# Performance work log

Hardware: AMD Instinct MI355X
Metric: run time of the kernel (lower is better)

The kernel has to match this reference:

```python
import jax, jax.numpy as jnp
import numpy as np

B, S, N, M, D = 1, 8, 768, 768, 64
K, RATIO, IT, THR = 8, 0.6, 16, 0.75
R_N, R_M = int(RATIO * N), int(RATIO * M)


def _solver(sx, sy, sm):
    # mask-weighted cross-correlation model: (Bi, D, D)
    w = sm.astype(sx.dtype)
    num = jnp.einsum('bnd,bnm,bme->bde', sx, w, sy)
    den = jnp.sum(w, axis=(-2, -1))[:, None, None] + 1e-6
    return num / den


def _evaluator(models, x, y, mask):
    # squared L2 residual ||x @ model - y||^2, NaN where mask is False -> (Bi, N, M)
    xt = jnp.einsum('bnd,bde->bne', x, models)
    sq = (jnp.sum(xt * xt, -1)[:, :, None] + jnp.sum(y * y, -1)[:, None, :]
          - 2.0 * jnp.einsum('bne,bme->bnm', xt, y))
    return jnp.where(mask, sq, jnp.nan)


def _ransac(x, y, mask, perm1, perm2):
    Bi, n, d = x.shape
    m = y.shape[1]
    p1 = perm1.reshape(-1)  # (IT*R_N,) values in [0, R_N)
    p2 = perm2.reshape(-1)
    s_x = x[:, p1].reshape(Bi * IT, R_N, d)
    s_y = y[:, p2].reshape(Bi * IT, R_M, d)
    s_m = mask[:, p1].reshape(Bi, IT, R_N, m)
    s_m = jnp.take_along_axis(s_m, perm2[None, :, None, :], axis=-1)
    s_m = s_m.reshape(Bi * IT, R_N, R_M)
    models = _solver(s_x, s_y, s_m)  # (Bi*IT, D, D)
    xr = jnp.broadcast_to(x[:, None], (Bi, IT, n, d)).reshape(Bi * IT, n, d)
    yr = jnp.broadcast_to(y[:, None], (Bi, IT, m, d)).reshape(Bi * IT, m, d)
    mr = jnp.broadcast_to(mask[:, None], (Bi, IT, n, m)).reshape(Bi * IT, n, m)
    errors = _evaluator(models, xr, yr, mr).reshape(Bi, IT, n, m)
    models = models.reshape(Bi, IT, D, D)
    avg = jnp.nanmean(errors, axis=(-1, -2))  # (Bi, IT)
    best = jnp.argmin(avg, axis=-1)
    best_model = jnp.take_along_axis(models, best[:, None, None, None], axis=1)[:, 0]
    best_errors = jnp.take_along_axis(errors, best[:, None, None, None], axis=1)[:, 0]
    thrs = jnp.nanquantile(best_errors, THR, axis=-1, keepdims=True)
    inliers = best_errors < thrs
    return best_model, inliers, best_errors


def _forward(qk, kks, qmask, kmask, perm1, perm2):
    mask = qmask & kmask  # (B*S, N, M)
    x = jnp.broadcast_to(qk[:, None], (B, S, N, D)).reshape(B * S, N, D)
    y = kks.reshape(B * S, M, D)
    bm, inl, be = _ransac(x, y, mask, perm1, perm2)
    bm = bm.reshape(B, S, D, D)
    inl = inl.reshape(B, S, N, M)
    be = be.reshape(B, S, N, M)
    avg = jnp.nanmean(be, axis=(-2, -1))  # (B, S)
    topk_err, topk_idx = jax.lax.top_k(avg, K)  # torch.topk default: largest
    tm = jnp.take_along_axis(bm, topk_idx[:, :, None, None], axis=1)
    ti = jnp.take_along_axis(inl, topk_idx[:, :, None, None], axis=1)
    return ti, tm, topk_err


def setup_inputs() -> dict:
    key = jax.random.key(0)
    k1, k2, k3, k4, k5, k6 = jax.random.split(key, 6)
    qk = jax.random.normal(k1, (B, N, D), jnp.float32)
    kks = jax.random.normal(k2, (B, S, M, D), jnp.float32)
    qmask = jax.random.randint(k3, (B * S, N, M), 0, 2) > 0
    kmask = jax.random.randint(k4, (B * S, N, M), 0, 2) > 0
    # _batch_randperm: permutations of [0, r_n)
    perm1 = jnp.argsort(jax.random.uniform(k5, (IT, R_N)), axis=-1).astype(jnp.int32)
    perm2 = jnp.argsort(jax.random.uniform(k6, (IT, R_M)), axis=-1).astype(jnp.int32)
    return {"qk": qk, "kks": kks, "qmask": qmask, "kmask": kmask,
            "perm1": perm1, "perm2": perm2}


def reference(qk, kks, qmask, kmask, perm1, perm2):
    return _forward(qk, kks, qmask, kmask, perm1, perm2)
```

## Files before the change

### kernel.cpp

```cpp
#include <hip/hip_runtime.h>
#include <math.h>

#define NN 768
#define MM 768
#define DD 64
#define BI 8
#define RN 460
#define KTOP 8
#define MSPLIT 4

static constexpr size_t OFF_TI = 0;
static constexpr size_t OFF_TM = (size_t)KTOP * NN * MM;
static constexpr size_t OFF_TE = OFF_TM + (size_t)KTOP * DD * DD;

static constexpr size_t TP_OFF    = 0;
static constexpr size_t NUMP_OFF  = TP_OFF + (size_t)MSPLIT * BI * RN * DD;
static constexpr size_t MODEL_OFF = NUMP_OFF + (size_t)8 * BI * DD * DD;
static constexpr size_t XT_OFF    = MODEL_OFF + (size_t)BI * DD * DD;
static constexpr size_t ERR_OFF   = XT_OFF + (size_t)BI * NN * DD;
static constexpr size_t FLOATS_END = ERR_OFF + (size_t)BI * NN * MM;
static constexpr size_t ERRP_SUM_BYTE = FLOATS_END * 4;
static constexpr size_t ERRP_CNT_BYTE = ERRP_SUM_BYTE + 1152 * 4;
static constexpr size_t DENP_BYTE     = ERRP_CNT_BYTE + 1152 * 4;
static constexpr size_t ORD_BYTE      = DENP_BYTE + 256 * 4;
static constexpr size_t PM_BYTE       = ORD_BYTE + 32;

__device__ __forceinline__ int ldm(const void* p, int flag, size_t idx) {
  if (flag) return ((const int*)p)[idx] != 0;
  return ((const unsigned char*)p)[idx] != 0;
}

__global__ __launch_bounds__(256) void k_pack(
    const void* __restrict__ qm, const void* __restrict__ km,
    unsigned long long* __restrict__ pm) {
  __shared__ int flag_sh;
  int tid = threadIdx.x;
  if (tid == 0) flag_sh = 0;
  __syncthreads();
  const unsigned* qw = (const unsigned*)qm;
  int f = 0;
  for (int i = tid; i < 1024; i += 256)
    if (qw[i] & 0xFFFFFF00u) f = 1;
  if (__ballot(f) && (tid & 63) == 0) atomicOr(&flag_sh, 1);
  __syncthreads();
  int flag = flag_sh ? 0 : 1;
  int b = blockIdx.y;
  int i = blockIdx.x * 4 + (tid >> 6);
  int lane = tid & 63;
  size_t row = ((size_t)b * NN + i) * MM;
  size_t prow = ((size_t)b * NN + i) * 16;
#pragma unroll
  for (int w = 0; w < 12; w++) {
    int j = w * 64 + lane;
    int ms = ldm(qm, flag, row + j) & ldm(km, flag, row + j);
    unsigned long long bl = __ballot(ms);
    if (lane == 0) pm[prow + w] = bl;
  }
}

__global__ __launch_bounds__(256) void k_tgemm(
    const float* __restrict__ kks, const unsigned long long* __restrict__ pm,
    float* __restrict__ tpart, int* __restrict__ denp) {
  __shared__ float ys[64 * 68];
  __shared__ int cnt_sh[4];
  int ntile = blockIdx.x;
  int split = blockIdx.y;
  int b = blockIdx.z;
  int tid = threadIdx.x;
  int e = tid & 63, g = tid >> 6;
  int n0 = ntile * 64 + g * 16;
  const float* yb = kks + (size_t)b * MM * DD;
  float acc[16];
#pragma unroll
  for (int i = 0; i < 16; i++) acc[i] = 0.f;
  int cnt = 0;
  for (int c = split * 2; c < split * 2 + 2; c++) {
    int m0 = c * 64;
    __syncthreads();
    for (int q = tid; q < 1024; q += 256) {
      int r = q >> 4, col = (q & 15) * 4;
      *(float4*)&ys[r * 68 + col] = *(const float4*)&yb[(size_t)(m0 + r) * DD + col];
    }
    __syncthreads();
    unsigned wlo[16], whi[16];
#pragma unroll
    for (int i = 0; i < 16; i++) {
      unsigned long long w = pm[((size_t)b * NN + (n0 + i)) * 16 + c];
      if (c == 7) w &= 0xFFFULL;
      wlo[i] = (unsigned)w;
      whi[i] = (unsigned)(w >> 32);
      if (n0 + i < RN) cnt += __builtin_popcountll(w);
    }
#pragma unroll 4
    for (int m = 0; m < 32; m++) {
      float yv = ys[m * 68 + e];
      int yi = __float_as_int(yv);
#pragma unroll
      for (int i = 0; i < 16; i++) {
        int sel = ((int)(wlo[i] << (31 - m))) >> 31;
        acc[i] += __int_as_float(yi & sel);
      }
    }
#pragma unroll 4
    for (int m = 0; m < 32; m++) {
      float yv = ys[(m + 32) * 68 + e];
      int yi = __float_as_int(yv);
#pragma unroll
      for (int i = 0; i < 16; i++) {
        int sel = ((int)(whi[i] << (31 - m))) >> 31;
        acc[i] += __int_as_float(yi & sel);
      }
    }
  }
#pragma unroll
  for (int i = 0; i < 16; i++) {
    int n = n0 + i;
    if (n < RN)
      tpart[(((size_t)split * BI + b) * RN + n) * DD + e] = acc[i];
  }
  if (e == 0) cnt_sh[g] = cnt;
  __syncthreads();
  if (tid == 0)
    denp[b * 32 + split * 8 + ntile] = cnt_sh[0] + cnt_sh[1] + cnt_sh[2] + cnt_sh[3];
}

__global__ __launch_bounds__(256) void k_num(
    const float* __restrict__ qk, const float* __restrict__ tpart, float* __restrict__ numpart) {
  __shared__ float xs[16 * 64];
  __shared__ float ts[16 * 64];
  int b = blockIdx.y;
  int c0 = blockIdx.x * 64;
  int tid = threadIdx.x;
  int e = tid & 63, dg = tid >> 6;
  float acc[16];
#pragma unroll
  for (int i = 0; i < 16; i++) acc[i] = 0.f;
  for (int it = 0; it < 4; it++) {
    int base = c0 + it * 16;
    for (int l = tid; l < 1024; l += 256) {
      int r = l >> 6, col = l & 63;
      int n = base + r;
      float tv = 0.f, xv = 0.f;
      if (n < RN) {
        xv = qk[(size_t)n * DD + col];
#pragma unroll
        for (int s = 0; s < MSPLIT; s++)
          tv += tpart[(((size_t)s * BI + b) * RN + n) * DD + col];
      }
      xs[l] = xv;
      ts[l] = tv;
    }
    __syncthreads();
#pragma unroll 4
    for (int r = 0; r < 16; r++) {
      float tv = ts[r * 64 + e];
#pragma unroll
      for (int i = 0; i < 16; i++) acc[i] += xs[r * 64 + dg + i * 4] * tv;
    }
    __syncthreads();
  }
#pragma unroll
  for (int i = 0; i < 16; i++) {
    int d = dg + i * 4;
    numpart[((size_t)blockIdx.x * BI + b) * (DD * DD) + (size_t)d * DD + e] = acc[i];
  }
}

__global__ __launch_bounds__(256) void k_model(
    const float* __restrict__ numpart, const int* __restrict__ denp, float* __restrict__ model) {
  __shared__ float inv_sh;
  int b = blockIdx.x;
  int tid = threadIdx.x;
  if (tid < 64) {
    int v = (tid < 32) ? denp[b * 32 + tid] : 0;
#pragma unroll
    for (int o = 32; o > 0; o >>= 1) v += __shfl_xor(v, o);
    if (tid == 0) inv_sh = 1.f / ((float)v + 1e-6f);
  }
  __syncthreads();
  float inv = inv_sh;
  for (int l = tid; l < DD * DD; l += 256) {
    float s = 0.f;
#pragma unroll
    for (int c = 0; c < 8; c++) s += numpart[((size_t)c * BI + b) * (DD * DD) + l];
    model[(size_t)b * DD * DD + l] = s * inv;
  }
}

__global__ __launch_bounds__(256) void k_xt(
    const float* __restrict__ qk, const float* __restrict__ model, float* __restrict__ xt) {
  __shared__ float ml[DD * DD];
  int b = blockIdx.y;
  int tid = threadIdx.x;
  for (int l = tid; l < DD * DD; l += 256) ml[l] = model[(size_t)b * DD * DD + l];
  __syncthreads();
  int n = blockIdx.x * 4 + (tid >> 6);
  int lane = tid & 63;
  float acc = 0.f;
#pragma unroll 8
  for (int d = 0; d < DD; d++) acc += qk[(size_t)n * DD + d] * ml[d * DD + lane];
  xt[((size_t)b * NN + n) * DD + lane] = acc;
}

__global__ __launch_bounds__(256) void k_err(
    const float* __restrict__ xt, const float* __restrict__ kks,
    const unsigned long long* __restrict__ pm,
    float* __restrict__ err, float* __restrict__ errp_sum, int* __restrict__ errp_cnt) {
  __shared__ float As[64 * 68];
  __shared__ float Bs[64 * 68];
  __shared__ float xx_s[64], yy_s[64];
  __shared__ float rsum[256];
  __shared__ int rcnt[256];
  int b = blockIdx.z;
  int wj = blockIdx.x;
  int i0 = blockIdx.y * 64, j0 = wj * 64;
  int tid = threadIdx.x;
  int tx = tid & 15, ty = tid >> 4;
  const float* xb = xt + ((size_t)b * NN + i0) * DD;
  const float* yb = kks + ((size_t)b * MM + j0) * DD;
  for (int q = tid; q < 1024; q += 256) {
    int r = q >> 4, c = q & 15;
    float4 va = ((const float4*)(xb + (size_t)r * DD))[c];
    float4 vb = ((const float4*)(yb + (size_t)r * DD))[c];
    *(float4*)&As[r * 68 + c * 4] = va;
    *(float4*)&Bs[r * 68 + c * 4] = vb;
  }
  __syncthreads();
  if (tid < 64) {
    float s = 0.f;
#pragma unroll 8
    for (int k2 = 0; k2 < 64; k2++) { float v = As[tid * 68 + k2]; s += v * v; }
    xx_s[tid] = s;
  } else if (tid < 128) {
    int r = tid - 64;
    float s = 0.f;
#pragma unroll 8
    for (int k2 = 0; k2 < 64; k2++) { float v = Bs[r * 68 + k2]; s += v * v; }
    yy_s[r] = s;
  }
  __syncthreads();
  float acc[4][4];
#pragma unroll
  for (int ii = 0; ii < 4; ii++)
#pragma unroll
    for (int jj = 0; jj < 4; jj++) acc[ii][jj] = 0.f;
  for (int k2 = 0; k2 < 64; k2 += 4) {
    float4 av[4], bv[4];
#pragma unroll
    for (int ii = 0; ii < 4; ii++) av[ii] = *(const float4*)&As[(ty + 16 * ii) * 68 + k2];
#pragma unroll
    for (int jj = 0; jj < 4; jj++) bv[jj] = *(const float4*)&Bs[(tx + 16 * jj) * 68 + k2];
#pragma unroll
    for (int ii = 0; ii < 4; ii++)
#pragma unroll
      for (int jj = 0; jj < 4; jj++)
        acc[ii][jj] += av[ii].x * bv[jj].x + av[ii].y * bv[jj].y +
                       av[ii].z * bv[jj].z + av[ii].w * bv[jj].w;
  }
  const float INF = __builtin_inff();
  float psum = 0.f;
  int pcnt = 0;
#pragma unroll
  for (int ii = 0; ii < 4; ii++) {
    int i = i0 + ty + 16 * ii;
    unsigned long long word = pm[((size_t)b * NN + i) * 16 + wj];
#pragma unroll
    for (int jj = 0; jj < 4; jj++) {
      int j = j0 + tx + 16 * jj;
      size_t idx = ((size_t)b * NN + i) * MM + j;
      int ms = (int)((word >> (tx + 16 * jj)) & 1ULL);
      float v = xx_s[ty + 16 * ii] + yy_s[tx + 16 * jj] - 2.f * acc[ii][jj];
      if (ms) { err[idx] = v; psum += v; pcnt++; }
      else    { err[idx] = INF; }
    }
  }
  rsum[tid] = psum;
  rcnt[tid] = pcnt;
  __syncthreads();
  for (int s = 128; s > 0; s >>= 1) {
    if (tid < s) { rsum[tid] += rsum[tid + s]; rcnt[tid] += rcnt[tid + s]; }
    __syncthreads();
  }
  if (tid == 0) {
    int blk = b * 144 + blockIdx.y * 12 + wj;
    errp_sum[blk] = rsum[0];
    errp_cnt[blk] = rcnt[0];
  }
}

__global__ __launch_bounds__(256) void k_rank(
    const float* __restrict__ errp_sum, const int* __restrict__ errp_cnt,
    const float* __restrict__ model, int* __restrict__ order, float* __restrict__ out) {
  __shared__ float red[256];
  __shared__ int redi[256];
  __shared__ float avg_sh[BI];
  __shared__ int ord_s[BI];
  int tid = threadIdx.x;
  for (int b = 0; b < BI; b++) {
    red[tid] = (tid < 144) ? errp_sum[b * 144 + tid] : 0.f;
    redi[tid] = (tid < 144) ? errp_cnt[b * 144 + tid] : 0;
    __syncthreads();
    for (int s = 128; s > 0; s >>= 1) {
      if (tid < s) { red[tid] += red[tid + s]; redi[tid] += redi[tid + s]; }
      __syncthreads();
    }
    if (tid == 0) avg_sh[b] = red[0] / (float)redi[0];
    __syncthreads();
  }
  if (tid == 0) {
    bool used[BI];
    for (int b = 0; b < BI; b++) used[b] = false;
    for (int k = 0; k < KTOP; k++) {
      int best = -1;
      float bv = -__builtin_inff();
      for (int b = 0; b < BI; b++)
        if (!used[b] && avg_sh[b] > bv) { bv = avg_sh[b]; best = b; }
      used[best] = true;
      ord_s[k] = best;
      order[k] = best;
      out[OFF_TE + k] = avg_sh[best];
    }
  }
  __syncthreads();
  for (int l = tid; l < KTOP * DD * DD; l += 256) {
    int k = l >> 12;
    out[OFF_TM + l] = model[(size_t)ord_s[k] * DD * DD + (l & (DD * DD - 1))];
  }
}

__device__ __forceinline__ unsigned f2key(float f) {
  unsigned u = __float_as_uint(f);
  return (u & 0x80000000u) ? ~u : (u | 0x80000000u);
}
__device__ __forceinline__ float key2f(unsigned k) {
  unsigned u = (k & 0x80000000u) ? (k ^ 0x80000000u) : ~k;
  return __uint_as_float(u);
}

__global__ __launch_bounds__(256) void k_quant(
    const float* __restrict__ err, const int* __restrict__ order, float* __restrict__ out) {
  int kk = blockIdx.y;
  int n = blockIdx.x * 4 + (threadIdx.x >> 6);
  int lane = threadIdx.x & 63;
  int b = order[kk];
  const float* row = err + ((size_t)b * NN + n) * MM;
  const float INF = __builtin_inff();
  float v[12];
  unsigned key[12];
#pragma unroll
  for (int w = 0; w < 3; w++) {
    float4 f4 = ((const float4*)row)[w * 64 + lane];
    v[w * 4 + 0] = f4.x; v[w * 4 + 1] = f4.y; v[w * 4 + 2] = f4.z; v[w * 4 + 3] = f4.w;
  }
  int cnt = 0;
#pragma unroll
  for (int r = 0; r < 12; r++) {
    key[r] = f2key(v[r]);
    cnt += __builtin_popcountll(__ballot(v[r] < INF));
  }
  float thr;
  if (cnt == 0) {
    thr = -INF;
  } else {
    float pos = 0.75f * (float)(cnt - 1);
    int k0 = (int)pos;
    float f = pos - (float)k0;
    unsigned lo = 0u, hi = 0xFFFFFFFFu;
    int target = k0 + 1;
    while (lo < hi) {
      unsigned mid = lo + ((hi - lo) >> 1);
      int c = 0;
#pragma unroll
      for (int r = 0; r < 12; r++) c += __builtin_popcountll(__ballot(key[r] <= mid));
      if (c >= target) hi = mid; else lo = mid + 1;
    }
    unsigned ka = lo;
    float a = key2f(ka);
    float b2;
    if (k0 + 1 >= cnt) {
      b2 = a;
    } else {
      int c1 = 0;
#pragma unroll
      for (int r = 0; r < 12; r++) c1 += __builtin_popcountll(__ballot(key[r] <= ka));
      if (c1 >= k0 + 2) {
        b2 = a;
      } else {
        unsigned mn = 0xFFFFFFFFu;
#pragma unroll
        for (int r = 0; r < 12; r++) mn = min(mn, (key[r] > ka) ? key[r] : 0xFFFFFFFFu);
#pragma unroll
        for (int off = 32; off > 0; off >>= 1) {
          unsigned o = (unsigned)__shfl_xor((int)mn, off);
          mn = min(mn, o);
        }
        b2 = key2f(mn);
      }
    }
    thr = a + f * (b2 - a);
  }
  float* orow = out + OFF_TI + ((size_t)kk * NN + n) * MM;
#pragma unroll
  for (int w = 0; w < 3; w++) {
    float4 o;
    o.x = (v[w * 4 + 0] < thr) ? 1.f : 0.f;
    o.y = (v[w * 4 + 1] < thr) ? 1.f : 0.f;
    o.z = (v[w * 4 + 2] < thr) ? 1.f : 0.f;
    o.w = (v[w * 4 + 3] < thr) ? 1.f : 0.f;
    ((float4*)orow)[w * 64 + lane] = o;
  }
}

extern "C" void kernel_launch(void* const* d_in, const int* in_sizes, int n_in,
                              void* d_out, int out_size, void* d_ws, size_t ws_size,
                              hipStream_t stream) {
  (void)in_sizes; (void)n_in; (void)out_size; (void)ws_size;
  const float* qk  = (const float*)d_in[0];
  const float* kks = (const float*)d_in[1];
  const void*  qm  = d_in[2];
  const void*  km  = d_in[3];
  float* out = (float*)d_out;

  float* wsf = (float*)d_ws;
  char*  wsb = (char*)d_ws;
  float* tpart   = wsf + TP_OFF;
  float* numpart = wsf + NUMP_OFF;
  float* model   = wsf + MODEL_OFF;
  float* xtb     = wsf + XT_OFF;
  float* errb    = wsf + ERR_OFF;
  float* errp_sum = (float*)(wsb + ERRP_SUM_BYTE);
  int* errp_cnt = (int*)(wsb + ERRP_CNT_BYTE);
  int* denp  = (int*)(wsb + DENP_BYTE);
  int* order = (int*)(wsb + ORD_BYTE);
  unsigned long long* pm = (unsigned long long*)(wsb + PM_BYTE);

  k_pack<<<dim3(NN / 4, BI), 256, 0, stream>>>(qm, km, pm);
  k_tgemm<<<dim3(8, MSPLIT, BI), 256, 0, stream>>>(kks, pm, tpart, denp);
  k_num<<<dim3(8, BI), 256, 0, stream>>>(qk, tpart, numpart);
  k_model<<<BI, 256, 0, stream>>>(numpart, denp, model);
  k_xt<<<dim3(NN / 4, BI), 256, 0, stream>>>(qk, model, xtb);
  k_err<<<dim3(MM / 64, NN / 64, BI), 256, 0, stream>>>(xtb, kks, pm, errb, errp_sum, errp_cnt);
  k_rank<<<1, 256, 0, stream>>>(errp_sum, errp_cnt, model, order, out);
  k_quant<<<dim3(NN / 4, KTOP), 256, 0, stream>>>(errb, order, out);
}
```

Measured before the change: 215.9 us.

## Fuse all eight stages into one cooperative persistent kernel with grid syncs

Replaces the eight separate kernel launches with a single cooperative kernel of 256 blocks that runs each stage in turn, separated by grid-wide syncs. A fallback relaunches the same stage code as separate kernels if cooperative launch fails. Work is redistributed to fit the fixed grid: the T-GEMM is split over all 8 column chunks and the numerator over 32 row chunks. The aim is to remove per-launch overhead and tail gaps between small kernels. The cost is that the heavy error and quantile stages now run on only 256 blocks, and seven grid barriers are added.

```diff
diff --git a/kernel.cpp b/kernel.cpp
--- a/kernel.cpp
+++ b/kernel.cpp
@@ -1,5 +1,8 @@
 #include <hip/hip_runtime.h>
+#include <hip/hip_cooperative_groups.h>
 #include <math.h>
+
+namespace cg = cooperative_groups;
 
 #define NN 768
 #define MM 768
@@ -7,327 +10,31 @@
 #define BI 8
 #define RN 460
 #define KTOP 8
-#define MSPLIT 4
+#define GRID 256
 
 static constexpr size_t OFF_TI = 0;
 static constexpr size_t OFF_TM = (size_t)KTOP * NN * MM;
 static constexpr size_t OFF_TE = OFF_TM + (size_t)KTOP * DD * DD;
 
 static constexpr size_t TP_OFF    = 0;
-static constexpr size_t NUMP_OFF  = TP_OFF + (size_t)MSPLIT * BI * RN * DD;
-static constexpr size_t MODEL_OFF = NUMP_OFF + (size_t)8 * BI * DD * DD;
+static constexpr size_t NUMP_OFF  = TP_OFF + (size_t)8 * BI * RN * DD;
+static constexpr size_t MODEL_OFF = NUMP_OFF + (size_t)32 * BI * DD * DD;
 static constexpr size_t XT_OFF    = MODEL_OFF + (size_t)BI * DD * DD;
 static constexpr size_t ERR_OFF   = XT_OFF + (size_t)BI * NN * DD;
-static constexpr size_t FLOATS_END = ERR_OFF + (size_t)BI * NN * MM;
-static constexpr size_t ERRP_SUM_BYTE = FLOATS_END * 4;
-static constexpr size_t ERRP_CNT_BYTE = ERRP_SUM_BYTE + 1152 * 4;
-static constexpr size_t DENP_BYTE     = ERRP_CNT_BYTE + 1152 * 4;
-static constexpr size_t ORD_BYTE      = DENP_BYTE + 256 * 4;
-static constexpr size_t PM_BYTE       = ORD_BYTE + 32;
+static constexpr size_t FEND      = ERR_OFF + (size_t)BI * NN * MM;
+static constexpr size_t ESUM_B = FEND * 4;
+static constexpr size_t ECNT_B = ESUM_B + 1152 * 4;
+static constexpr size_t DENP_B = ECNT_B + 1152 * 4;
+static constexpr size_t ORD_B  = DENP_B + 512 * 4;
+static constexpr size_t PM_B   = ORD_B + 64;
+
+static constexpr int SM_BYTES = 37392;
 
 __device__ __forceinline__ int ldm(const void* p, int flag, size_t idx) {
   if (flag) return ((const int*)p)[idx] != 0;
   return ((const unsigned char*)p)[idx] != 0;
 }
 
-__global__ __launch_bounds__(256) void k_pack(
-    const void* __restrict__ qm, const void* __restrict__ km,
-    unsigned long long* __restrict__ pm) {
-  __shared__ int flag_sh;
-  int tid = threadIdx.x;
-  if (tid == 0) flag_sh = 0;
-  __syncthreads();
-  const unsigned* qw = (const unsigned*)qm;
-  int f = 0;
-  for (int i = tid; i < 1024; i += 256)
-    if (qw[i] & 0xFFFFFF00u) f = 1;
-  if (__ballot(f) && (tid & 63) == 0) atomicOr(&flag_sh, 1);
-  __syncthreads();
-  int flag = flag_sh ? 0 : 1;
-  int b = blockIdx.y;
-  int i = blockIdx.x * 4 + (tid >> 6);
-  int lane = tid & 63;
-  size_t row = ((size_t)b * NN + i) * MM;
-  size_t prow = ((size_t)b * NN + i) * 16;
-#pragma unroll
-  for (int w = 0; w < 12; w++) {
-    int j = w * 64 + lane;
-    int ms = ldm(qm, flag, row + j) & ldm(km, flag, row + j);
-    unsigned long long bl = __ballot(ms);
-    if (lane == 0) pm[prow + w] = bl;
-  }
-}
-
-__global__ __launch_bounds__(256) void k_tgemm(
-    const float* __restrict__ kks, const unsigned long long* __restrict__ pm,
-    float* __restrict__ tpart, int* __restrict__ denp) {
-  __shared__ float ys[64 * 68];
-  __shared__ int cnt_sh[4];
-  int ntile = blockIdx.x;
-  int split = blockIdx.y;
-  int b = blockIdx.z;
-  int tid = threadIdx.x;
-  int e = tid & 63, g = tid >> 6;
-  int n0 = ntile * 64 + g * 16;
-  const float* yb = kks + (size_t)b * MM * DD;
-  float acc[16];
-#pragma unroll
-  for (int i = 0; i < 16; i++) acc[i] = 0.f;
-  int cnt = 0;
-  for (int c = split * 2; c < split * 2 + 2; c++) {
-    int m0 = c * 64;
-    __syncthreads();
-    for (int q = tid; q < 1024; q += 256) {
-      int r = q >> 4, col = (q & 15) * 4;
-      *(float4*)&ys[r * 68 + col] = *(const float4*)&yb[(size_t)(m0 + r) * DD + col];
-    }
-    __syncthreads();
-    unsigned wlo[16], whi[16];
-#pragma unroll
-    for (int i = 0; i < 16; i++) {
-      unsigned long long w = pm[((size_t)b * NN + (n0 + i)) * 16 + c];
-      if (c == 7) w &= 0xFFFULL;
-      wlo[i] = (unsigned)w;
-      whi[i] = (unsigned)(w >> 32);
-      if (n0 + i < RN) cnt += __builtin_popcountll(w);
-    }
-#pragma unroll 4
-    for (int m = 0; m < 32; m++) {
-      float yv = ys[m * 68 + e];
-      int yi = __float_as_int(yv);
-#pragma unroll
-      for (int i = 0; i < 16; i++) {
-        int sel = ((int)(wlo[i] << (31 - m))) >> 31;
-        acc[i] += __int_as_float(yi & sel);
-      }
-    }
-#pragma unroll 4
-    for (int m = 0; m < 32; m++) {
-      float yv = ys[(m + 32) * 68 + e];
-      int yi = __float_as_int(yv);
-#pragma unroll
-      for (int i = 0; i < 16; i++) {
-        int sel = ((int)(whi[i] << (31 - m))) >> 31;
-        acc[i] += __int_as_float(yi & sel);
-      }
-    }
-  }
-#pragma unroll
-  for (int i = 0; i < 16; i++) {
-    int n = n0 + i;
-    if (n < RN)
-      tpart[(((size_t)split * BI + b) * RN + n) * DD + e] = acc[i];
-  }
-  if (e == 0) cnt_sh[g] = cnt;
-  __syncthreads();
-  if (tid == 0)
-    denp[b * 32 + split * 8 + ntile] = cnt_sh[0] + cnt_sh[1] + cnt_sh[2] + cnt_sh[3];
-}
-
-__global__ __launch_bounds__(256) void k_num(
-    const float* __restrict__ qk, const float* __restrict__ tpart, float* __restrict__ numpart) {
-  __shared__ float xs[16 * 64];
-  __shared__ float ts[16 * 64];
-  int b = blockIdx.y;
-  int c0 = blockIdx.x * 64;
-  int tid = threadIdx.x;
-  int e = tid & 63, dg = tid >> 6;
-  float acc[16];
-#pragma unroll
-  for (int i = 0; i < 16; i++) acc[i] = 0.f;
-  for (int it = 0; it < 4; it++) {
-    int base = c0 + it * 16;
-    for (int l = tid; l < 1024; l += 256) {
-      int r = l >> 6, col = l & 63;
-      int n = base + r;
-      float tv = 0.f, xv = 0.f;
-      if (n < RN) {
-        xv = qk[(size_t)n * DD + col];
-#pragma unroll
-        for (int s = 0; s < MSPLIT; s++)
-          tv += tpart[(((size_t)s * BI + b) * RN + n) * DD + col];
-      }
-      xs[l] = xv;
-      ts[l] = tv;
-    }
-    __syncthreads();
-#pragma unroll 4
-    for (int r = 0; r < 16; r++) {
-      float tv = ts[r * 64 + e];
-#pragma unroll
-      for (int i = 0; i < 16; i++) acc[i] += xs[r * 64 + dg + i * 4] * tv;
-    }
-    __syncthreads();
-  }
-#pragma unroll
-  for (int i = 0; i < 16; i++) {
-    int d = dg + i * 4;
-    numpart[((size_t)blockIdx.x * BI + b) * (DD * DD) + (size_t)d * DD + e] = acc[i];
-  }
-}
-
-__global__ __launch_bounds__(256) void k_model(
-    const float* __restrict__ numpart, const int* __restrict__ denp, float* __restrict__ model) {
-  __shared__ float inv_sh;
-  int b = blockIdx.x;
-  int tid = threadIdx.x;
-  if (tid < 64) {
-    int v = (tid < 32) ? denp[b * 32 + tid] : 0;
-#pragma unroll
-    for (int o = 32; o > 0; o >>= 1) v += __shfl_xor(v, o);
-    if (tid == 0) inv_sh = 1.f / ((float)v + 1e-6f);
-  }
-  __syncthreads();
-  float inv = inv_sh;
-  for (int l = tid; l < DD * DD; l += 256) {
-    float s = 0.f;
-#pragma unroll
-    for (int c = 0; c < 8; c++) s += numpart[((size_t)c * BI + b) * (DD * DD) + l];
-    model[(size_t)b * DD * DD + l] = s * inv;
-  }
-}
-
-__global__ __launch_bounds__(256) void k_xt(
-    const float* __restrict__ qk, const float* __restrict__ model, float* __restrict__ xt) {
-  __shared__ float ml[DD * DD];
-  int b = blockIdx.y;
-  int tid = threadIdx.x;
-  for (int l = tid; l < DD * DD; l += 256) ml[l] = model[(size_t)b * DD * DD + l];
-  __syncthreads();
-  int n = blockIdx.x * 4 + (tid >> 6);
-  int lane = tid & 63;
-  float acc = 0.f;
-#pragma unroll 8
-  for (int d = 0; d < DD; d++) acc += qk[(size_t)n * DD + d] * ml[d * DD + lane];
-  xt[((size_t)b * NN + n) * DD + lane] = acc;
-}
-
-__global__ __launch_bounds__(256) void k_err(
-    const float* __restrict__ xt, const float* __restrict__ kks,
-    const unsigned long long* __restrict__ pm,
-    float* __restrict__ err, float* __restrict__ errp_sum, int* __restrict__ errp_cnt) {
-  __shared__ float As[64 * 68];
-  __shared__ float Bs[64 * 68];
-  __shared__ float xx_s[64], yy_s[64];
-  __shared__ float rsum[256];
-  __shared__ int rcnt[256];
-  int b = blockIdx.z;
-  int wj = blockIdx.x;
-  int i0 = blockIdx.y * 64, j0 = wj * 64;
-  int tid = threadIdx.x;
-  int tx = tid & 15, ty = tid >> 4;
-  const float* xb = xt + ((size_t)b * NN + i0) * DD;
-  const float* yb = kks + ((size_t)b * MM + j0) * DD;
-  for (int q = tid; q < 1024; q += 256) {
-    int r = q >> 4, c = q & 15;
-    float4 va = ((const float4*)(xb + (size_t)r * DD))[c];
-    float4 vb = ((const float4*)(yb + (size_t)r * DD))[c];
-    *(float4*)&As[r * 68 + c * 4] = va;
-    *(float4*)&Bs[r * 68 + c * 4] = vb;
-  }
-  __syncthreads();
-  if (tid < 64) {
-    float s = 0.f;
-#pragma unroll 8
-    for (int k2 = 0; k2 < 64; k2++) { float v = As[tid * 68 + k2]; s += v * v; }
-    xx_s[tid] = s;
-  } else if (tid < 128) {
-    int r = tid - 64;
-    float s = 0.f;
-#pragma unroll 8
-    for (int k2 = 0; k2 < 64; k2++) { float v = Bs[r * 68 + k2]; s += v * v; }
-    yy_s[r] = s;
-  }
-  __syncthreads();
-  float acc[4][4];
-#pragma unroll
-  for (int ii = 0; ii < 4; ii++)
-#pragma unroll
-    for (int jj = 0; jj < 4; jj++) acc[ii][jj] = 0.f;
-  for (int k2 = 0; k2 < 64; k2 += 4) {
-    float4 av[4], bv[4];
-#pragma unroll
-    for (int ii = 0; ii < 4; ii++) av[ii] = *(const float4*)&As[(ty + 16 * ii) * 68 + k2];
-#pragma unroll
-    for (int jj = 0; jj < 4; jj++) bv[jj] = *(const float4*)&Bs[(tx + 16 * jj) * 68 + k2];
-#pragma unroll
-    for (int ii = 0; ii < 4; ii++)
-#pragma unroll
-      for (int jj = 0; jj < 4; jj++)
-        acc[ii][jj] += av[ii].x * bv[jj].x + av[ii].y * bv[jj].y +
-                       av[ii].z * bv[jj].z + av[ii].w * bv[jj].w;
-  }
-  const float INF = __builtin_inff();
-  float psum = 0.f;
-  int pcnt = 0;
-#pragma unroll
-  for (int ii = 0; ii < 4; ii++) {
-    int i = i0 + ty + 16 * ii;
-    unsigned long long word = pm[((size_t)b * NN + i) * 16 + wj];
-#pragma unroll
-    for (int jj = 0; jj < 4; jj++) {
-      int j = j0 + tx + 16 * jj;
-      size_t idx = ((size_t)b * NN + i) * MM + j;
-      int ms = (int)((word >> (tx + 16 * jj)) & 1ULL);
-      float v = xx_s[ty + 16 * ii] + yy_s[tx + 16 * jj] - 2.f * acc[ii][jj];
-      if (ms) { err[idx] = v; psum += v; pcnt++; }
-      else    { err[idx] = INF; }
-    }
-  }
-  rsum[tid] = psum;
-  rcnt[tid] = pcnt;
-  __syncthreads();
-  for (int s = 128; s > 0; s >>= 1) {
-    if (tid < s) { rsum[tid] += rsum[tid + s]; rcnt[tid] += rcnt[tid + s]; }
-    __syncthreads();
-  }
-  if (tid == 0) {
-    int blk = b * 144 + blockIdx.y * 12 + wj;
-    errp_sum[blk] = rsum[0];
-    errp_cnt[blk] = rcnt[0];
-  }
-}
-
-__global__ __launch_bounds__(256) void k_rank(
-    const float* __restrict__ errp_sum, const int* __restrict__ errp_cnt,
-    const float* __restrict__ model, int* __restrict__ order, float* __restrict__ out) {
-  __shared__ float red[256];
-  __shared__ int redi[256];
-  __shared__ float avg_sh[BI];
-  __shared__ int ord_s[BI];
-  int tid = threadIdx.x;
-  for (int b = 0; b < BI; b++) {
-    red[tid] = (tid < 144) ? errp_sum[b * 144 + tid] : 0.f;
-    redi[tid] = (tid < 144) ? errp_cnt[b * 144 + tid] : 0;
-    __syncthreads();
-    for (int s = 128; s > 0; s >>= 1) {
-      if (tid < s) { red[tid] += red[tid + s]; redi[tid] += redi[tid + s]; }
-      __syncthreads();
-    }
-    if (tid == 0) avg_sh[b] = red[0] / (float)redi[0];
-    __syncthreads();
-  }
-  if (tid == 0) {
-    bool used[BI];
-    for (int b = 0; b < BI; b++) used[b] = false;
-    for (int k = 0; k < KTOP; k++) {
-      int best = -1;
-      float bv = -__builtin_inff();
-      for (int b = 0; b < BI; b++)
-        if (!used[b] && avg_sh[b] > bv) { bv = avg_sh[b]; best = b; }
-      used[best] = true;
-      ord_s[k] = best;
-      order[k] = best;
-      out[OFF_TE + k] = avg_sh[best];
-    }
-  }
-  __syncthreads();
-  for (int l = tid; l < KTOP * DD * DD; l += 256) {
-    int k = l >> 12;
-    out[OFF_TM + l] = model[(size_t)ord_s[k] * DD * DD + (l & (DD * DD - 1))];
-  }
-}
-
 __device__ __forceinline__ unsigned f2key(float f) {
   unsigned u = __float_as_uint(f);
   return (u & 0x80000000u) ? ~u : (u | 0x80000000u);
@@ -337,78 +44,405 @@
   return __uint_as_float(u);
 }
 
-__global__ __launch_bounds__(256) void k_quant(
-    const float* __restrict__ err, const int* __restrict__ order, float* __restrict__ out) {
-  int kk = blockIdx.y;
-  int n = blockIdx.x * 4 + (threadIdx.x >> 6);
-  int lane = threadIdx.x & 63;
-  int b = order[kk];
-  const float* row = err + ((size_t)b * NN + n) * MM;
+__device__ void stage_run(
+    int stage, int bid, int tid,
+    const float* __restrict__ qk, const float* __restrict__ kks,
+    const void* __restrict__ qm, const void* __restrict__ km,
+    float* __restrict__ out, float* __restrict__ wsf, char* smem, int flag) {
+  const int lane = tid & 63, g = tid >> 6;
+  char* wsb = (char*)wsf;
+  float* tpart   = wsf + TP_OFF;
+  float* numpart = wsf + NUMP_OFF;
+  float* model   = wsf + MODEL_OFF;
+  float* xtb     = wsf + XT_OFF;
+  float* errb    = wsf + ERR_OFF;
+  float* esum = (float*)(wsb + ESUM_B);
+  int*   ecnt = (int*)(wsb + ECNT_B);
+  int*   denp = (int*)(wsb + DENP_B);
+  int*   ordw = (int*)(wsb + ORD_B);
+  unsigned long long* pmw = (unsigned long long*)(wsb + PM_B);
   const float INF = __builtin_inff();
-  float v[12];
-  unsigned key[12];
-#pragma unroll
-  for (int w = 0; w < 3; w++) {
-    float4 f4 = ((const float4*)row)[w * 64 + lane];
-    v[w * 4 + 0] = f4.x; v[w * 4 + 1] = f4.y; v[w * 4 + 2] = f4.z; v[w * 4 + 3] = f4.w;
-  }
-  int cnt = 0;
-#pragma unroll
-  for (int r = 0; r < 12; r++) {
-    key[r] = f2key(v[r]);
-    cnt += __builtin_popcountll(__ballot(v[r] < INF));
-  }
-  float thr;
-  if (cnt == 0) {
-    thr = -INF;
-  } else {
-    float pos = 0.75f * (float)(cnt - 1);
-    int k0 = (int)pos;
-    float f = pos - (float)k0;
-    unsigned lo = 0u, hi = 0xFFFFFFFFu;
-    int target = k0 + 1;
-    while (lo < hi) {
-      unsigned mid = lo + ((hi - lo) >> 1);
-      int c = 0;
-#pragma unroll
-      for (int r = 0; r < 12; r++) c += __builtin_popcountll(__ballot(key[r] <= mid));
-      if (c >= target) hi = mid; else lo = mid + 1;
-    }
-    unsigned ka = lo;
-    float a = key2f(ka);
-    float b2;
-    if (k0 + 1 >= cnt) {
-      b2 = a;
-    } else {
-      int c1 = 0;
-#pragma unroll
-      for (int r = 0; r < 12; r++) c1 += __builtin_popcountll(__ballot(key[r] <= ka));
-      if (c1 >= k0 + 2) {
-        b2 = a;
+
+  switch (stage) {
+  case 1: {
+    int b = bid >> 5, seg = bid & 31;
+    for (int rr = 0; rr < 6; rr++) {
+      int n = seg * 24 + g * 6 + rr;
+      size_t rowb = ((size_t)b * NN + n) * MM;
+      size_t prow = ((size_t)b * NN + n) * 12;
+#pragma unroll
+      for (int w = 0; w < 12; w++) {
+        int j = w * 64 + lane;
+        int cm = ldm(qm, flag, rowb + j) & ldm(km, flag, rowb + j);
+        unsigned long long bl = __ballot(cm);
+        if (lane == 0) pmw[prow + w] = bl;
+      }
+    }
+    break;
+  }
+  case 2: {
+    float* ys = (float*)smem;
+    int* cntsh = (int*)(smem + 17408);
+    for (int u = bid; u < 512; u += GRID) {
+      int b = u >> 6, c = (u >> 3) & 7, ntile = u & 7;
+      int m0 = c * 64, n0 = ntile * 64 + g * 16;
+      const float* yb = kks + (size_t)b * MM * DD;
+      __syncthreads();
+      for (int q = tid; q < 1024; q += 256) {
+        int r = q >> 4, col = (q & 15) * 4;
+        *(float4*)&ys[r * 68 + col] = *(const float4*)&yb[(size_t)(m0 + r) * DD + col];
+      }
+      unsigned wlo[16], whi[16];
+      int cnt = 0;
+#pragma unroll
+      for (int i = 0; i < 16; i++) {
+        int n = n0 + i;
+        unsigned long long w = pmw[((size_t)b * NN + n) * 12 + c];
+        if (c == 7) w &= 0xFFFULL;
+        wlo[i] = (unsigned)w; whi[i] = (unsigned)(w >> 32);
+        if (n < RN) cnt += __builtin_popcountll(w);
+      }
+      __syncthreads();
+      float acc[16];
+#pragma unroll
+      for (int i = 0; i < 16; i++) acc[i] = 0.f;
+#pragma unroll 4
+      for (int m = 0; m < 32; m++) {
+        int yi = __float_as_int(ys[m * 68 + lane]);
+#pragma unroll
+        for (int i = 0; i < 16; i++) {
+          int sel = ((int)(wlo[i] << (31 - m))) >> 31;
+          acc[i] += __int_as_float(yi & sel);
+        }
+      }
+#pragma unroll 4
+      for (int m = 0; m < 32; m++) {
+        int yi = __float_as_int(ys[(m + 32) * 68 + lane]);
+#pragma unroll
+        for (int i = 0; i < 16; i++) {
+          int sel = ((int)(whi[i] << (31 - m))) >> 31;
+          acc[i] += __int_as_float(yi & sel);
+        }
+      }
+#pragma unroll
+      for (int i = 0; i < 16; i++) {
+        int n = n0 + i;
+        if (n < RN)
+          tpart[(((size_t)c * BI + b) * RN + n) * DD + lane] = acc[i];
+      }
+      if (lane == 0) cntsh[g] = cnt;
+      __syncthreads();
+      if (tid == 0) denp[u] = cntsh[0] + cntsh[1] + cntsh[2] + cntsh[3];
+    }
+    break;
+  }
+  case 3: {
+    float* xs = (float*)smem;
+    float* ts = (float*)(smem + 4096);
+    int chunk = bid >> 3, b = bid & 7;
+    for (int l = tid; l < 1024; l += 256) {
+      int r = l >> 6, col = l & 63;
+      int n = chunk * 16 + r;
+      float xv = 0.f, tv = 0.f;
+      if (n < RN) {
+        xv = qk[(size_t)n * DD + col];
+#pragma unroll
+        for (int cc = 0; cc < 8; cc++)
+          tv += tpart[(((size_t)cc * BI + b) * RN + n) * DD + col];
+      }
+      xs[l] = xv; ts[l] = tv;
+    }
+    __syncthreads();
+    float acc[16];
+#pragma unroll
+    for (int i = 0; i < 16; i++) acc[i] = 0.f;
+#pragma unroll 4
+    for (int r = 0; r < 16; r++) {
+      float tv = ts[r * 64 + lane];
+#pragma unroll
+      for (int i = 0; i < 16; i++) acc[i] += xs[r * 64 + g + i * 4] * tv;
+    }
+#pragma unroll
+    for (int i = 0; i < 16; i++)
+      numpart[((size_t)chunk * BI + b) * (DD * DD) + (size_t)(g + i * 4) * DD + lane] = acc[i];
+    break;
+  }
+  case 4: {
+    if (bid < 64) {
+      float* invp = (float*)smem;
+      int b = bid >> 3, part = bid & 7;
+      if (tid < 64) {
+        int v = denp[b * 64 + tid];
+#pragma unroll
+        for (int o = 32; o > 0; o >>= 1) v += __shfl_xor(v, o);
+        if (tid == 0) invp[0] = 1.f / ((float)v + 1e-6f);
+      }
+      __syncthreads();
+      float inv = invp[0];
+      for (int l = part * 512 + tid; l < part * 512 + 512; l += 256) {
+        float s = 0.f;
+#pragma unroll
+        for (int cc = 0; cc < 32; cc++) s += numpart[((size_t)cc * BI + b) * (DD * DD) + l];
+        model[(size_t)b * (DD * DD) + l] = s * inv;
+      }
+    }
+    break;
+  }
+  case 5: {
+    float* ml = (float*)smem;
+    int b = bid >> 5, seg = bid & 31;
+    const float4* msrc = (const float4*)(model + (size_t)b * DD * DD);
+    for (int q = tid; q < 1024; q += 256) ((float4*)ml)[q] = msrc[q];
+    __syncthreads();
+#pragma unroll
+    for (int rr = 0; rr < 6; rr++) {
+      int n = seg * 24 + g * 6 + rr;
+      float acc = 0.f;
+#pragma unroll 8
+      for (int d = 0; d < DD; d++) acc += qk[(size_t)n * DD + d] * ml[d * DD + lane];
+      xtb[((size_t)b * NN + n) * DD + lane] = acc;
+    }
+    break;
+  }
+  case 6: {
+    float* As = (float*)smem;
+    float* Bs = (float*)(smem + 17408);
+    float* xx = (float*)(smem + 34816);
+    float* yy = (float*)(smem + 35072);
+    float* rsum = (float*)(smem + 35328);
+    int* rcnt = (int*)(smem + 36352);
+    int tx = tid & 15, ty = tid >> 4;
+    for (int t = bid; t < 1152; t += GRID) {
+      int b = t / 144, rem = t % 144;
+      int i0 = (rem / 12) * 64, wj = rem % 12, j0 = wj * 64;
+      __syncthreads();
+      const float* xb = xtb + ((size_t)b * NN + i0) * DD;
+      const float* yb = kks + ((size_t)b * MM + j0) * DD;
+      for (int q = tid; q < 1024; q += 256) {
+        int r = q >> 4, c = q & 15;
+        *(float4*)&As[r * 68 + c * 4] = ((const float4*)(xb + (size_t)r * DD))[c];
+        *(float4*)&Bs[r * 68 + c * 4] = ((const float4*)(yb + (size_t)r * DD))[c];
+      }
+      __syncthreads();
+      if (tid < 64) {
+        float s = 0.f;
+#pragma unroll 8
+        for (int k2 = 0; k2 < 64; k2++) { float v = As[tid * 68 + k2]; s += v * v; }
+        xx[tid] = s;
+      } else if (tid < 128) {
+        int r = tid - 64;
+        float s = 0.f;
+#pragma unroll 8
+        for (int k2 = 0; k2 < 64; k2++) { float v = Bs[r * 68 + k2]; s += v * v; }
+        yy[r] = s;
+      }
+      __syncthreads();
+      float acc[4][4];
+#pragma unroll
+      for (int ii = 0; ii < 4; ii++)
+#pragma unroll
+        for (int jj = 0; jj < 4; jj++) acc[ii][jj] = 0.f;
+      for (int k2 = 0; k2 < 64; k2 += 4) {
+        float4 av[4], bv[4];
+#pragma unroll
+        for (int ii = 0; ii < 4; ii++) av[ii] = *(const float4*)&As[(ty + 16 * ii) * 68 + k2];
+#pragma unroll
+        for (int jj = 0; jj < 4; jj++) bv[jj] = *(const float4*)&Bs[(tx + 16 * jj) * 68 + k2];
+#pragma unroll
+        for (int ii = 0; ii < 4; ii++)
+#pragma unroll
+          for (int jj = 0; jj < 4; jj++)
+            acc[ii][jj] += av[ii].x * bv[jj].x + av[ii].y * bv[jj].y +
+                           av[ii].z * bv[jj].z + av[ii].w * bv[jj].w;
+      }
+      float psum = 0.f;
+      int pcnt = 0;
+#pragma unroll
+      for (int ii = 0; ii < 4; ii++) {
+        int i = i0 + ty + 16 * ii;
+        unsigned long long word = pmw[((size_t)b * NN + i) * 12 + wj];
+        size_t rowb = ((size_t)b * NN + i) * MM;
+#pragma unroll
+        for (int jj = 0; jj < 4; jj++) {
+          int j = j0 + tx + 16 * jj;
+          int cm = (int)((word >> (tx + 16 * jj)) & 1ULL);
+          float v = xx[ty + 16 * ii] + yy[tx + 16 * jj] - 2.f * acc[ii][jj];
+          if (cm) { errb[rowb + j] = v; psum += v; pcnt++; }
+          else    { errb[rowb + j] = INF; }
+        }
+      }
+      rsum[tid] = psum;
+      rcnt[tid] = pcnt;
+      __syncthreads();
+      for (int s = 128; s > 0; s >>= 1) {
+        if (tid < s) { rsum[tid] += rsum[tid + s]; rcnt[tid] += rcnt[tid + s]; }
+        __syncthreads();
+      }
+      if (tid == 0) { esum[t] = rsum[0]; ecnt[t] = rcnt[0]; }
+    }
+    break;
+  }
+  case 7: {
+    if (bid == 0) {
+      float* red = (float*)smem;
+      int* redi = (int*)(smem + 1024);
+      float* avg = (float*)(smem + 2048);
+      int* ords = (int*)(smem + 2080);
+      for (int b = 0; b < BI; b++) {
+        red[tid] = (tid < 144) ? esum[b * 144 + tid] : 0.f;
+        redi[tid] = (tid < 144) ? ecnt[b * 144 + tid] : 0;
+        __syncthreads();
+        for (int s = 128; s > 0; s >>= 1) {
+          if (tid < s) { red[tid] += red[tid + s]; redi[tid] += redi[tid + s]; }
+          __syncthreads();
+        }
+        if (tid == 0) avg[b] = red[0] / (float)redi[0];
+        __syncthreads();
+      }
+      if (tid == 0) {
+        bool used[BI];
+        for (int b = 0; b < BI; b++) used[b] = false;
+        for (int k = 0; k < KTOP; k++) {
+          int best = -1;
+          float bv = -INF;
+          for (int b = 0; b < BI; b++)
+            if (!used[b] && avg[b] > bv) { bv = avg[b]; best = b; }
+          used[best] = true;
+          ords[k] = best;
+          ordw[k] = best;
+          out[OFF_TE + k] = avg[best];
+        }
+      }
+      __syncthreads();
+      for (int l = tid; l < KTOP * DD * DD; l += 256) {
+        int k = l >> 12;
+        out[OFF_TM + l] = model[(size_t)ords[k] * DD * DD + (l & (DD * DD - 1))];
+      }
+    }
+    break;
+  }
+  case 8: {
+    int kk = bid >> 5, seg = bid & 31;
+    int b = ordw[kk];
+    for (int rr = 0; rr < 6; rr++) {
+      int n = seg * 24 + g * 6 + rr;
+      const float* row = errb + ((size_t)b * NN + n) * MM;
+      float v[12];
+      unsigned key[12];
+#pragma unroll
+      for (int w = 0; w < 3; w++) {
+        float4 f4 = ((const float4*)row)[w * 64 + lane];
+        v[w * 4 + 0] = f4.x; v[w * 4 + 1] = f4.y; v[w * 4 + 2] = f4.z; v[w * 4 + 3] = f4.w;
+      }
+      int cnt = 0;
+#pragma unroll
+      for (int r = 0; r < 12; r++) {
+        key[r] = f2key(v[r]);
+        cnt += __builtin_popcountll(__ballot(v[r] < INF));
+      }
+      float thr;
+      if (cnt == 0) {
+        thr = -INF;
       } else {
-        unsigned mn = 0xFFFFFFFFu;
-#pragma unroll
-        for (int r = 0; r < 12; r++) mn = min(mn, (key[r] > ka) ? key[r] : 0xFFFFFFFFu);
-#pragma unroll
-        for (int off = 32; off > 0; off >>= 1) {
-          unsigned o = (unsigned)__shfl_xor((int)mn, off);
-          mn = min(mn, o);
-        }
-        b2 = key2f(mn);
-      }
-    }
-    thr = a + f * (b2 - a);
-  }
-  float* orow = out + OFF_TI + ((size_t)kk * NN + n) * MM;
-#pragma unroll
-  for (int w = 0; w < 3; w++) {
-    float4 o;
-    o.x = (v[w * 4 + 0] < thr) ? 1.f : 0.f;
-    o.y = (v[w * 4 + 1] < thr) ? 1.f : 0.f;
-    o.z = (v[w * 4 + 2] < thr) ? 1.f : 0.f;
-    o.w = (v[w * 4 + 3] < thr) ? 1.f : 0.f;
-    ((float4*)orow)[w * 64 + lane] = o;
-  }
+        float pos = 0.75f * (float)(cnt - 1);
+        int k0 = (int)pos;
+        float f = pos - (float)k0;
+        unsigned lo = 0u, hi = 0xFFFFFFFFu;
+        int target = k0 + 1;
+        while (lo < hi) {
+          unsigned mid = lo + ((hi - lo) >> 1);
+          int c = 0;
+#pragma unroll
+          for (int r = 0; r < 12; r++) c += __builtin_popcountll(__ballot(key[r] <= mid));
+          if (c >= target) hi = mid; else lo = mid + 1;
+        }
+        unsigned ka = lo;
+        float a = key2f(ka);
+        float b2;
+        if (k0 + 1 >= cnt) {
+          b2 = a;
+        } else {
+          int c1 = 0;
+#pragma unroll
+          for (int r = 0; r < 12; r++) c1 += __builtin_popcountll(__ballot(key[r] <= ka));
+          if (c1 >= k0 + 2) {
+            b2 = a;
+          } else {
+            unsigned mn = 0xFFFFFFFFu;
+#pragma unroll
+            for (int r = 0; r < 12; r++) mn = min(mn, (key[r] > ka) ? key[r] : 0xFFFFFFFFu);
+#pragma unroll
+            for (int off = 32; off > 0; off >>= 1) {
+              unsigned o = (unsigned)__shfl_xor((int)mn, off);
+              mn = min(mn, o);
+            }
+            b2 = key2f(mn);
+          }
+        }
+        thr = a + f * (b2 - a);
+      }
+      float* orow = out + OFF_TI + ((size_t)kk * NN + n) * MM;
+#pragma unroll
+      for (int w = 0; w < 3; w++) {
+        float4 o;
+        o.x = (v[w * 4 + 0] < thr) ? 1.f : 0.f;
+        o.y = (v[w * 4 + 1] < thr) ? 1.f : 0.f;
+        o.z = (v[w * 4 + 2] < thr) ? 1.f : 0.f;
+        o.w = (v[w * 4 + 3] < thr) ? 1.f : 0.f;
+        ((float4*)orow)[w * 64 + lane] = o;
+      }
+    }
+    break;
+  }
+  }
+}
+
+__device__ __forceinline__ int detect_flag(const void* qm, char* smem, int tid) {
+  int* flg = (int*)(smem + 37376);
+  const unsigned* qw = (const unsigned*)qm;
+  unsigned w = qw[tid];
+  unsigned long long any = __ballot((w & 0xFFFFFF00u) != 0);
+  if ((tid & 63) == 0) flg[tid >> 6] = (any != 0) ? 1 : 0;
+  __syncthreads();
+  int flag = (flg[0] | flg[1] | flg[2] | flg[3]) ? 0 : 1;
+  __syncthreads();
+  return flag;
+}
+
+__global__ __launch_bounds__(256) void mega(
+    const float* __restrict__ qk, const float* __restrict__ kks,
+    const void* __restrict__ qm, const void* __restrict__ km,
+    float* __restrict__ out, float* __restrict__ wsf) {
+  __shared__ __align__(16) char smem[SM_BYTES];
+  cg::grid_group grid = cg::this_grid();
+  int bid = blockIdx.x, tid = threadIdx.x;
+  int flag = detect_flag(qm, smem, tid);
+  stage_run(1, bid, tid, qk, kks, qm, km, out, wsf, smem, flag);
+  grid.sync();
+  stage_run(2, bid, tid, qk, kks, qm, km, out, wsf, smem, flag);
+  grid.sync();
+  stage_run(3, bid, tid, qk, kks, qm, km, out, wsf, smem, flag);
+  grid.sync();
+  stage_run(4, bid, tid, qk, kks, qm, km, out, wsf, smem, flag);
+  grid.sync();
+  stage_run(5, bid, tid, qk, kks, qm, km, out, wsf, smem, flag);
+  grid.sync();
+  stage_run(6, bid, tid, qk, kks, qm, km, out, wsf, smem, flag);
+  grid.sync();
+  stage_run(7, bid, tid, qk, kks, qm, km, out, wsf, smem, flag);
+  grid.sync();
+  stage_run(8, bid, tid, qk, kks, qm, km, out, wsf, smem, flag);
+}
+
+__global__ __launch_bounds__(256) void staged(
+    int stage,
+    const float* __restrict__ qk, const float* __restrict__ kks,
+    const void* __restrict__ qm, const void* __restrict__ km,
+    float* __restrict__ out, float* __restrict__ wsf) {
+  __shared__ __align__(16) char smem[SM_BYTES];
+  int bid = blockIdx.x, tid = threadIdx.x;
+  int flag = detect_flag(qm, smem, tid);
+  stage_run(stage, bid, tid, qk, kks, qm, km, out, wsf, smem, flag);
 }
 
 extern "C" void kernel_launch(void* const* d_in, const int* in_sizes, int n_in,
@@ -420,26 +454,13 @@
   const void*  qm  = d_in[2];
   const void*  km  = d_in[3];
   float* out = (float*)d_out;
-
   float* wsf = (float*)d_ws;
-  char*  wsb = (char*)d_ws;
-  float* tpart   = wsf + TP_OFF;
-  float* numpart = wsf + NUMP_OFF;
-  float* model   = wsf + MODEL_OFF;
-  float* xtb     = wsf + XT_OFF;
-  float* errb    = wsf + ERR_OFF;
-  float* errp_sum = (float*)(wsb + ERRP_SUM_BYTE);
-  int* errp_cnt = (int*)(wsb + ERRP_CNT_BYTE);
-  int* denp  = (int*)(wsb + DENP_BYTE);
-  int* order = (int*)(wsb + ORD_BYTE);
-  unsigned long long* pm = (unsigned long long*)(wsb + PM_BYTE);
-
-  k_pack<<<dim3(NN / 4, BI), 256, 0, stream>>>(qm, km, pm);
-  k_tgemm<<<dim3(8, MSPLIT, BI), 256, 0, stream>>>(kks, pm, tpart, denp);
-  k_num<<<dim3(8, BI), 256, 0, stream>>>(qk, tpart, numpart);
-  k_model<<<BI, 256, 0, stream>>>(numpart, denp, model);
-  k_xt<<<dim3(NN / 4, BI), 256, 0, stream>>>(qk, model, xtb);
-  k_err<<<dim3(MM / 64, NN / 64, BI), 256, 0, stream>>>(xtb, kks, pm, errb, errp_sum, errp_cnt);
-  k_rank<<<1, 256, 0, stream>>>(errp_sum, errp_cnt, model, order, out);
-  k_quant<<<dim3(NN / 4, KTOP), 256, 0, stream>>>(errb, order, out);
-}
+  void* args[] = {(void*)&qk, (void*)&kks, (void*)&qm, (void*)&km, (void*)&out, (void*)&wsf};
+  hipError_t e = hipLaunchCooperativeKernel(reinterpret_cast<const void*>(&mega),
+                                            dim3(GRID), dim3(256), args, 0, stream);
+  if (e != hipSuccess) {
+    (void)hipGetLastError();
+    for (int s = 1; s <= 8; s++)
+      staged<<<dim3(GRID), dim3(256), 0, stream>>>(s, qk, kks, qm, km, out, wsf);
+  }
+}
```

Measured after the change: 490.4 us. 127% more time.
